# Kernel optimization log

Hardware: AMD Instinct MI355X
Metric: run time of the kernel (lower is better)

The kernel has to match this reference:

```python
import jax, jax.numpy as jnp
import numpy as np
from functools import partial

D = 512      # world_state_dim
M = 1000     # memory_size
H = 8        # attention heads
DH = D // H  # head dim
EPS = 1e-5


def _layernorm(x, g, b):
    mu = jnp.mean(x, axis=-1, keepdims=True)
    var = jnp.mean((x - mu) ** 2, axis=-1, keepdims=True)
    return (x - mu) * jax.lax.rsqrt(var + EPS) * g + b


def setup_inputs() -> dict:
    key = jax.random.key(0)
    ks = jax.random.split(key, 24)
    B = 8192
    w = lambda k, shp: (jax.random.normal(k, shp, dtype=jnp.float32) * 0.02)
    inp = {
        "observations": jax.random.normal(ks[0], (B, D), dtype=jnp.float32),
        "ego_motion": jax.random.normal(ks[1], (B, 16), dtype=jnp.float32),
        "world_memory": jax.random.normal(ks[2], (M, D), dtype=jnp.float32) * 0.1,
        # encoder: Linear(D,D) -> ReLU -> LN(D) -> Linear(D,D)
        "enc_w1": w(ks[3], (D, D)), "enc_b1": jnp.zeros((D,), jnp.float32),
        "enc_g": jnp.ones((D,), jnp.float32), "enc_beta": jnp.zeros((D,), jnp.float32),
        "enc_w2": w(ks[4], (D, D)), "enc_b2": jnp.zeros((D,), jnp.float32),
        # multihead attention in/out projections
        "wq": w(ks[5], (D, D)), "bq": jnp.zeros((D,), jnp.float32),
        "wk": w(ks[6], (D, D)), "bk": jnp.zeros((D,), jnp.float32),
        "wv": w(ks[7], (D, D)), "bv": jnp.zeros((D,), jnp.float32),
        "wo": w(ks[8], (D, D)), "bo": jnp.zeros((D,), jnp.float32),
        # transition: Linear(D+16,D) -> ReLU -> LN(D) -> Linear(D,D)
        "tr_w1": w(ks[9], (D, D + 16)), "tr_b1": jnp.zeros((D,), jnp.float32),
        "tr_g": jnp.ones((D,), jnp.float32), "tr_beta": jnp.zeros((D,), jnp.float32),
        "tr_w2": w(ks[10], (D, D)), "tr_b2": jnp.zeros((D,), jnp.float32),
        # quality head: Linear(D,128) -> ReLU -> Linear(128,1) -> Sigmoid
        "q_w1": w(ks[11], (128, D)), "q_b1": jnp.zeros((128,), jnp.float32),
        "q_w2": w(ks[12], (1, 128)), "q_b2": jnp.zeros((1,), jnp.float32),
        # random slots for memory-bank scatter-EMA update (replaces torch.randint)
        "update_indices": jax.random.randint(ks[13], (B,), 0, M, dtype=jnp.int32),
    }
    return inp


def _forward_core(observations, ego_motion, world_memory,
                  enc_w1, enc_b1, enc_g, enc_beta, enc_w2, enc_b2,
                  wq, bq, wk, bk, wv, bv, wo, bo,
                  tr_w1, tr_b1, tr_g, tr_beta, tr_w2, tr_b2,
                  q_w1, q_b1, q_w2, q_b2):
    B = observations.shape[0]
    # world_encoder
    h = jax.nn.relu(observations @ enc_w1.T + enc_b1)
    encoded = _layernorm(h, enc_g, enc_beta) @ enc_w2.T + enc_b2  # [B, D]
    # cross-attention: one query per batch row over shared memory bank
    q = (encoded @ wq.T + bq).reshape(B, H, DH)
    k = (world_memory @ wk.T + bk).reshape(M, H, DH)  # shared across batch
    v = (world_memory @ wv.T + bv).reshape(M, H, DH)
    scores = jnp.einsum("bhd,mhd->bhm", q, k) / jnp.sqrt(jnp.float32(DH))
    attn = jax.nn.softmax(scores, axis=-1)              # [B, H, M]
    ctx = jnp.einsum("bhm,mhd->bhd", attn, v).reshape(B, D)
    memory_states = ctx @ wo.T + bo
    # fuse + transition
    fused = 0.7 * encoded + 0.3 * memory_states
    x = jnp.concatenate([fused, ego_motion], axis=-1)   # [B, D+16]
    h2 = jax.nn.relu(x @ tr_w1.T + tr_b1)
    next_state = _layernorm(h2, tr_g, tr_beta) @ tr_w2.T + tr_b2  # [B, D]
    # quality head
    qh = jax.nn.relu(next_state @ q_w1.T + q_b1)
    quality = jax.nn.sigmoid(qh @ q_w2.T + q_b2)        # [B, 1]
    mem_weights = jnp.mean(attn, axis=1)                # [B, M] avg over heads
    return next_state, quality, mem_weights


def _update_memory_bank(world_memory, next_state, quality, update_indices):
    # Sequential scatter-EMA, faithful to the torch loop (duplicates compound).
    mask = quality[:, 0] > 0.7

    def step(mem, inp):
        idx, st, m = inp
        row = mem[idx]
        new_row = jnp.where(m, 0.9 * row + 0.1 * st, row)
        return mem.at[idx].set(new_row), None

    updated, _ = jax.lax.scan(step, world_memory, (update_indices, next_state, mask))
    return updated


@jax.jit
def reference(observations, ego_motion, world_memory,
              enc_w1, enc_b1, enc_g, enc_beta, enc_w2, enc_b2,
              wq, bq, wk, bk, wv, bv, wo, bo,
              tr_w1, tr_b1, tr_g, tr_beta, tr_w2, tr_b2,
              q_w1, q_b1, q_w2, q_b2, update_indices):
    next_state, quality, mem_weights = _forward_core(
        observations, ego_motion, world_memory,
        enc_w1, enc_b1, enc_g, enc_beta, enc_w2, enc_b2,
        wq, bq, wk, bk, wv, bv, wo, bo,
        tr_w1, tr_b1, tr_g, tr_beta, tr_w2, tr_b2,
        q_w1, q_b1, q_w2, q_b2)
    updated_memory = _update_memory_bank(world_memory, next_state, quality, update_indices)
    return next_state, quality, updated_memory
```

## Files before the change

kernel.cpp:

```cpp
#include <hip/hip_runtime.h>

#define B_ 8192
#define D_ 512
#define M_ 1000
#define H_ 8
#define LOG2E 1.4426950408889634f

typedef unsigned short u16;
typedef __attribute__((ext_vector_type(8))) short bf16x8;
typedef __attribute__((ext_vector_type(4))) float f32x4;

__device__ __forceinline__ float bf2f(u16 u) {
    union { unsigned u; float f; } c; c.u = ((unsigned)u) << 16; return c.f;
}
__device__ __forceinline__ u16 f2bf(float f) {
    union { float f; unsigned u; } c; c.f = f;
    unsigned r = (c.u + 0x7fffu + ((c.u >> 16) & 1u)) >> 16;
    return (u16)r;
}
__device__ __forceinline__ unsigned f2bf_fast_u(float f) {
    union { float f; unsigned u; } c; c.f = f;
    return (c.u + 0x8000u) >> 16;
}
__device__ __forceinline__ float wave_sum(float v) {
#pragma unroll
    for (int off = 32; off > 0; off >>= 1) v += __shfl_xor(v, off);
    return v;
}

template<bool RELU, bool WF32, bool VTOUT>
__device__ __forceinline__ void gemm_core(
    int bx, int by, u16* As, u16* Bs,
    const u16* __restrict__ A0, const u16* __restrict__ A1,
    const u16* __restrict__ A2, int lda0, int lda1, int lda2,
    const u16* __restrict__ W0, const u16* __restrict__ W1,
    const u16* __restrict__ W2, int ldw0, int ldw1, int ldw2,
    int kb1, int kb2,
    const float* __restrict__ bias, float bscale, float cscale,
    float* __restrict__ Cf, u16* __restrict__ Cb, u16* __restrict__ VT,
    int M, int N, int K, int ldc)
{
    const int m0 = by * 64, n0 = bx * 64;
    if (m0 >= M || n0 >= N) return;
    const int t = threadIdx.x, w = t >> 6, l = t & 63;
    const int wm = (w >> 1) * 32, wn = (w & 1) * 32;
    const int li = l & 15, quad = l >> 4;

    f32x4 acc[2][2];
#pragma unroll
    for (int i = 0; i < 2; ++i)
#pragma unroll
        for (int j = 0; j < 2; ++j) acc[i][j] = (f32x4){0.f, 0.f, 0.f, 0.f};

    for (int k0 = 0; k0 < K; k0 += 64) {
        const u16* Ab; const u16* Wb; int ldab, ldwb, ko;
        if (k0 < kb1)      { Ab = A0; ldab = lda0; Wb = W0; ldwb = ldw0; ko = k0; }
        else if (k0 < kb2) { Ab = A1; ldab = lda1; Wb = W1; ldwb = ldw1; ko = k0 - kb1; }
        else               { Ab = A2; ldab = lda2; Wb = W2; ldwb = ldw2; ko = k0 - kb2; }
#pragma unroll
        for (int i = 0; i < 2; ++i) {
            const int rl = w * 16 + i * 8 + (l >> 3);
            const int ck = (l & 7) ^ (rl & 7);
            int ga = m0 + rl; ga = ga < M ? ga : M - 1;
            __builtin_amdgcn_global_load_lds(
                (const __attribute__((address_space(1))) void*)(Ab + (size_t)ga * ldab + ko + ck * 8),
                (__attribute__((address_space(3))) void*)(As + (w * 16 + i * 8) * 64),
                16, 0, 0);
        }
#pragma unroll
        for (int i = 0; i < 2; ++i) {
            const int rl = w * 16 + i * 8 + (l >> 3);
            const int ck = (l & 7) ^ (rl & 7);
            int gb = n0 + rl; gb = gb < N ? gb : N - 1;
            __builtin_amdgcn_global_load_lds(
                (const __attribute__((address_space(1))) void*)(Wb + (size_t)gb * ldwb + ko + ck * 8),
                (__attribute__((address_space(3))) void*)(Bs + (w * 16 + i * 8) * 64),
                16, 0, 0);
        }
        __syncthreads();
#pragma unroll
        for (int ks = 0; ks < 2; ++ks) {
            const int ch = ks * 4 + quad;
            bf16x8 af[2], bfr[2];
#pragma unroll
            for (int mt = 0; mt < 2; ++mt) {
                const int r = wm + mt * 16 + li;
                af[mt] = *(const bf16x8*)(As + r * 64 + ((ch ^ (r & 7)) * 8));
            }
#pragma unroll
            for (int nt = 0; nt < 2; ++nt) {
                const int r = wn + nt * 16 + li;
                bfr[nt] = *(const bf16x8*)(Bs + r * 64 + ((ch ^ (r & 7)) * 8));
            }
#pragma unroll
            for (int mt = 0; mt < 2; ++mt)
#pragma unroll
                for (int nt = 0; nt < 2; ++nt)
                    acc[mt][nt] = __builtin_amdgcn_mfma_f32_16x16x32_bf16(
                        af[mt], bfr[nt], acc[mt][nt], 0, 0, 0);
        }
        __syncthreads();
    }

    float bv[2];
#pragma unroll
    for (int nt = 0; nt < 2; ++nt) bv[nt] = bias[n0 + wn + nt * 16 + li] * bscale;
#pragma unroll
    for (int mt = 0; mt < 2; ++mt) {
        const int row0 = m0 + wm + mt * 16 + quad * 4;
#pragma unroll
        for (int nt = 0; nt < 2; ++nt) {
            const int col = n0 + wn + nt * 16 + li;
            if (VTOUT && col >= 512) {
                ushort4 pk;
                u16 pv[4];
#pragma unroll
                for (int r = 0; r < 4; ++r) {
                    float v = acc[mt][nt][r] * cscale + bv[nt];
                    pv[r] = (row0 + r < M_) ? f2bf(v) : (u16)0;
                }
                pk.x = pv[0]; pk.y = pv[1]; pk.z = pv[2]; pk.w = pv[3];
                *(ushort4*)(VT + (size_t)(col - 512) * 1024 + row0) = pk;
            } else {
#pragma unroll
                for (int r = 0; r < 4; ++r) {
                    const int row = row0 + r;
                    if (row >= M) continue;
                    float v = acc[mt][nt][r] * cscale + bv[nt];
                    if (RELU) v = fmaxf(v, 0.f);
                    Cb[(size_t)row * ldc + col] = f2bf(v);
                    if (WF32) Cf[(size_t)row * ldc + col] = v;
                }
            }
        }
    }
}

template<bool RELU, bool WF32>
__launch_bounds__(256)
__global__ void mgemm(const u16* __restrict__ A0, const u16* __restrict__ A1,
                      const u16* __restrict__ A2, int lda0, int lda1, int lda2,
                      const u16* __restrict__ W0, const u16* __restrict__ W1,
                      const u16* __restrict__ W2, int ldw0, int ldw1, int ldw2,
                      int kb1, int kb2,
                      const float* __restrict__ bias, float bscale, float cscale,
                      float* __restrict__ Cf, u16* __restrict__ Cb,
                      int M, int N, int K, int ldc)
{
    __shared__ u16 As[64 * 64];
    __shared__ u16 Bs[64 * 64];
    gemm_core<RELU, WF32, false>(blockIdx.x, blockIdx.y, As, Bs,
                                 A0, A1, A2, lda0, lda1, lda2,
                                 W0, W1, W2, ldw0, ldw1, ldw2, kb1, kb2,
                                 bias, bscale, cscale, Cf, Cb, nullptr, M, N, K, ldc);
}

__launch_bounds__(256)
__global__ void megagemm(const u16* __restrict__ obs_bf, const u16* __restrict__ w_enc1,
                         const float* __restrict__ enc_b1, u16* __restrict__ hbuf,
                         const u16* __restrict__ wmem_bf, const u16* __restrict__ w_k,
                         const float* __restrict__ bkv, u16* __restrict__ KVbuf,
                         u16* __restrict__ VTb,
                         const u16* __restrict__ w_q, const u16* __restrict__ w_tr1,
                         const u16* __restrict__ w_e2t, const u16* __restrict__ w_wot,
                         u16* __restrict__ w_qe, u16* __restrict__ w_ae,
                         u16* __restrict__ w_co)
{
    __shared__ u16 As[64 * 64];
    __shared__ u16 Bs[64 * 64];
    const int bx = blockIdx.x, by = blockIdx.y;
    if (blockIdx.z == 0) {
        gemm_core<true, false, false>(bx, by, As, Bs,
            obs_bf, obs_bf, obs_bf, 512, 512, 512,
            w_enc1, w_enc1, w_enc1, 512, 512, 512, 512, 512,
            enc_b1, 1.f, 1.f, nullptr, hbuf, nullptr, B_, 512, 512, 512);
    } else {
        if (by < 16) {
            gemm_core<false, false, true>(bx, by, As, Bs,
                wmem_bf, wmem_bf, wmem_bf, 512, 512, 512,
                w_k, w_k, w_k, 512, 512, 512, 512, 512,
                bkv, 1.f, 1.f, nullptr, KVbuf, VTb, 1024, 1024, 512, 1024);
        } else if (by < 24) {
            gemm_core<false, false, false>(bx, by - 16, As, Bs,
                w_q, w_q, w_q, 512, 512, 512,
                w_e2t, w_e2t, w_e2t, 512, 512, 512, 512, 512,
                bkv, 0.f, 1.0f, nullptr, w_qe, nullptr, 512, 512, 512, 512);
        } else if (by < 32) {
            gemm_core<false, false, false>(bx, by - 24, As, Bs,
                w_tr1, w_tr1, w_tr1, 576, 576, 576,
                w_e2t, w_e2t, w_e2t, 512, 512, 512, 512, 512,
                bkv, 0.f, 0.7f, nullptr, w_ae, nullptr, 512, 512, 512, 512);
        } else if (by < 40) {
            gemm_core<false, false, false>(bx, by - 32, As, Bs,
                w_tr1, w_tr1, w_tr1, 576, 576, 576,
                w_wot, w_wot, w_wot, 512, 512, 512, 512, 512,
                bkv, 0.f, 0.3f, nullptr, w_co, nullptr, 512, 512, 512, 512);
        }
    }
}

#define PADK 72

__launch_bounds__(256, 3)
__global__ void attn_kernel(const u16* __restrict__ Q, const u16* __restrict__ KV,
                            const u16* __restrict__ VT, u16* __restrict__ ctx)
{
    __shared__ u16 Ks[2][64 * 64];
    __shared__ u16 Vs[2][64 * 64];
    __shared__ u16 P[4 * 32 * PADK];
    const int t = threadIdx.x, w = t >> 6, l = t & 63;
    const int h = blockIdx.y;
    const int q0 = blockIdx.x * 128 + w * 32;
    u16* Pw = P + w * (32 * PADK);
    const int li = l & 15, quad = l >> 4;

    bf16x8 aq[2][2];
#pragma unroll
    for (int qnt = 0; qnt < 2; ++qnt)
#pragma unroll
        for (int ks = 0; ks < 2; ++ks) {
            const int row = q0 + qnt * 16 + li;
            aq[qnt][ks] = *(const bf16x8*)(Q + (size_t)row * 512 + h * 64 + ks * 32 + quad * 8);
        }

    bf16x8 ones;
#pragma unroll
    for (int i = 0; i < 8; ++i) ones[i] = (short)0x3F80;

    f32x4 oacc[2][4];
    f32x4 lacc[2];
#pragma unroll
    for (int mt = 0; mt < 2; ++mt) {
        lacc[mt] = (f32x4){0.f, 0.f, 0.f, 0.f};
#pragma unroll
        for (int nt = 0; nt < 4; ++nt) oacc[mt][nt] = (f32x4){0.f, 0.f, 0.f, 0.f};
    }

    auto stage = [&](int kc, int buf) {
#pragma unroll
        for (int i = 0; i < 2; ++i) {
            const int f = i * 256 + t;
            const int r = f >> 3;
            const int ck = (f & 7) ^ (r & 7);
            __builtin_amdgcn_global_load_lds(
                (const __attribute__((address_space(1))) void*)(KV + (size_t)(kc + r) * 1024 + h * 64 + ck * 8),
                (__attribute__((address_space(3))) void*)(&Ks[buf][f * 8]),
                16, 0, 0);
        }
#pragma unroll
        for (int i = 0; i < 2; ++i) {
            const int f = i * 256 + t;
            const int r = f >> 3;
            const int ck = (f & 7) ^ (r & 7);
            __builtin_amdgcn_global_load_lds(
                (const __attribute__((address_space(1))) void*)(VT + (size_t)(h * 64 + r) * 1024 + kc + ck * 8),
                (__attribute__((address_space(3))) void*)(&Vs[buf][f * 8]),
                16, 0, 0);
        }
    };

    stage(0, 0);
    for (int ic = 0; ic < 16; ++ic) {
        const int kc = ic * 64;
        __syncthreads();
        if (ic < 15) stage(kc + 64, (ic + 1) & 1);
        const u16* ksb = &Ks[ic & 1][0];
        const u16* vsb = &Vs[ic & 1][0];

        f32x4 s[4][2];
#pragma unroll
        for (int kmt = 0; kmt < 4; ++kmt)
#pragma unroll
            for (int qnt = 0; qnt < 2; ++qnt) s[kmt][qnt] = (f32x4){0.f, 0.f, 0.f, 0.f};
        __builtin_amdgcn_s_setprio(1);
#pragma unroll
        for (int ks = 0; ks < 2; ++ks) {
            const int ch = ks * 4 + quad;
            bf16x8 bk[4];
#pragma unroll
            for (int kmt = 0; kmt < 4; ++kmt) {
                const int key = kmt * 16 + li;
                bk[kmt] = *(const bf16x8*)(ksb + key * 64 + ((ch ^ (key & 7)) * 8));
            }
#pragma unroll
            for (int kmt = 0; kmt < 4; ++kmt)
#pragma unroll
                for (int qnt = 0; qnt < 2; ++qnt)
                    s[kmt][qnt] = __builtin_amdgcn_mfma_f32_16x16x32_bf16(
                        bk[kmt], aq[qnt][ks], s[kmt][qnt], 0, 0, 0);
        }
        __builtin_amdgcn_s_setprio(0);
        if (kc == 960) {
#pragma unroll
            for (int kmt = 2; kmt < 4; ++kmt)
#pragma unroll
                for (int r = 0; r < 4; ++r) {
                    const int key_local = kmt * 16 + quad * 4 + r;
                    if (960 + key_local >= M_) {
                        s[kmt][0][r] = -3.0e38f;
                        s[kmt][1][r] = -3.0e38f;
                    }
                }
        }
#pragma unroll
        for (int kmt = 0; kmt < 4; ++kmt)
#pragma unroll
            for (int qnt = 0; qnt < 2; ++qnt) {
                const unsigned b0 = f2bf_fast_u(exp2f(s[kmt][qnt][0]));
                const unsigned b1 = f2bf_fast_u(exp2f(s[kmt][qnt][1]));
                const unsigned b2w = f2bf_fast_u(exp2f(s[kmt][qnt][2]));
                const unsigned b3 = f2bf_fast_u(exp2f(s[kmt][qnt][3]));
                const int off = (qnt * 16 + li) * PADK + kmt * 16 + quad * 4;
                *(uint2*)(Pw + off) = make_uint2(b0 | (b1 << 16), b2w | (b3 << 16));
            }
        __builtin_amdgcn_s_setprio(1);
#pragma unroll
        for (int ks = 0; ks < 2; ++ks) {
            const int ch = ks * 4 + quad;
            bf16x8 ap[2];
#pragma unroll
            for (int mt = 0; mt < 2; ++mt)
                ap[mt] = *(const bf16x8*)(Pw + (mt * 16 + li) * PADK + ch * 8);
#pragma unroll
            for (int mt = 0; mt < 2; ++mt)
                lacc[mt] = __builtin_amdgcn_mfma_f32_16x16x32_bf16(
                    ap[mt], ones, lacc[mt], 0, 0, 0);
#pragma unroll
            for (int nt = 0; nt < 4; ++nt) {
                const int dh = nt * 16 + li;
                const bf16x8 bvv = *(const bf16x8*)(vsb + dh * 64 + ((ch ^ (dh & 7)) * 8));
#pragma unroll
                for (int mt = 0; mt < 2; ++mt)
                    oacc[mt][nt] = __builtin_amdgcn_mfma_f32_16x16x32_bf16(
                        ap[mt], bvv, oacc[mt][nt], 0, 0, 0);
            }
        }
        __builtin_amdgcn_s_setprio(0);
    }

#pragma unroll
    for (int mt = 0; mt < 2; ++mt)
#pragma unroll
        for (int r = 0; r < 4; ++r) {
            const int row = q0 + mt * 16 + quad * 4 + r;
            const float inv = 1.0f / lacc[mt][r];
#pragma unroll
            for (int nt = 0; nt < 4; ++nt)
                ctx[(size_t)row * 512 + h * 64 + nt * 16 + li] = f2bf(oacc[mt][nt][r] * inv);
        }
}

__launch_bounds__(256)
__global__ void ln_bf(u16* __restrict__ X, const float* __restrict__ g,
                      const float* __restrict__ be, int rows)
{
    const int row = blockIdx.x * 4 + (threadIdx.x >> 6);
    const int lane = threadIdx.x & 63;
    if (row >= rows) return;
    u16* p = X + (size_t)row * 512 + lane * 8;
    uint4 d = *(const uint4*)p;
    const unsigned dd[4] = {d.x, d.y, d.z, d.w};
    float v[8];
#pragma unroll
    for (int i = 0; i < 4; ++i) {
        v[2 * i]     = bf2f((u16)(dd[i] & 0xffffu));
        v[2 * i + 1] = bf2f((u16)(dd[i] >> 16));
    }
    float s = 0.f;
#pragma unroll
    for (int i = 0; i < 8; ++i) s += v[i];
    s = wave_sum(s);
    const float mu = s * (1.0f / 512.0f);
    float vs = 0.f;
#pragma unroll
    for (int i = 0; i < 8; ++i) { v[i] -= mu; vs += v[i] * v[i]; }
    vs = wave_sum(vs);
    const float r = rsqrtf(vs * (1.0f / 512.0f) + 1e-5f);
    const float* gp = g + lane * 8;
    const float* bp = be + lane * 8;
    unsigned o[4];
#pragma unroll
    for (int i = 0; i < 4; ++i) {
        const u16 lo = f2bf(v[2 * i] * r * gp[2 * i] + bp[2 * i]);
        const u16 hi = f2bf(v[2 * i + 1] * r * gp[2 * i + 1] + bp[2 * i + 1]);
        o[i] = (unsigned)lo | ((unsigned)hi << 16);
    }
    *(uint4*)p = make_uint4(o[0], o[1], o[2], o[3]);
}

__launch_bounds__(256)
__global__ void prep_all(const float* enc_w1, const float* wk_f, const float* wv_f,
                         const float* tr_w2, const float* q_w1, const float* wq,
                         const float* tr_w1, const float* enc_w2, const float* wo,
                         const float* obs, const float* wmem, const float* ego,
                         const float* bk, const float* bvv, const float* bq,
                         const float* enc_b2, const float* trb1, const float* bo,
                         u16* w_enc1, u16* w_k, u16* w_v, u16* w_tr2, u16* w_qh,
                         u16* w_q, u16* w_tr1, u16* w_e2t, u16* w_wot,
                         u16* obs_bf, u16* wmem_bf, u16* ego64,
                         float* bkv, float* bqe, float* btr)
{
    __shared__ float tl[64][65];
    const int seg = blockIdx.y;
    const int t = threadIdx.x;
    const int bx = blockIdx.x;

    if (seg <= 5) {
        const float* s; u16* d; int n; float sc = 1.0f;
        switch (seg) {
            case 0: s = enc_w1; d = w_enc1; n = 262144; break;
            case 1: s = wk_f;   d = w_k;    n = 262144; break;
            case 2: s = wv_f;   d = w_v;    n = 262144; break;
            case 3: s = tr_w2;  d = w_tr2;  n = 262144; break;
            case 4: s = q_w1;   d = w_qh;   n = 65536;  break;
            default: s = wq;    d = w_q;    n = 262144; sc = 0.125f * LOG2E; break;
        }
        const int i0 = (bx * 256 + t) * 4;
        if (i0 + 3 < n) {
            const float4 v = *(const float4*)(s + i0);
            ushort4 o;
            o.x = f2bf(v.x * sc); o.y = f2bf(v.y * sc);
            o.z = f2bf(v.z * sc); o.w = f2bf(v.w * sc);
            *(ushort4*)(d + i0) = o;
        }
    } else if (seg == 6) {
#pragma unroll
        for (int k = 0; k < 4; ++k) {
            const int i = (bx * 256 + t) * 4 + k;
            if (i < 294912) {
                const int r = i / 576, c = i - r * 576;
                w_tr1[i] = (c < 528) ? f2bf(tr_w1[r * 528 + c]) : (u16)0;
            }
        }
    } else if (seg <= 8) {
        if (bx >= 64) return;
        const float* S = (seg == 7) ? enc_w2 : wo;
        u16* D = (seg == 7) ? w_e2t : w_wot;
        const int r0 = (bx >> 3) * 64, c0 = (bx & 7) * 64;
#pragma unroll
        for (int i = 0; i < 16; ++i) {
            const int idx = t + i * 256;
            tl[idx >> 6][idx & 63] = S[(size_t)(r0 + (idx >> 6)) * 512 + c0 + (idx & 63)];
        }
        __syncthreads();
#pragma unroll
        for (int i = 0; i < 16; ++i) {
            const int idx = t + i * 256;
            const int c = idx >> 6, r = idx & 63;
            D[(size_t)(c0 + c) * 512 + r0 + r] = f2bf(tl[r][c]);
        }
    } else if (seg == 9) {
        const int nth = gridDim.x * 256;
        for (int i = bx * 256 + t; i < B_ * 512 / 4; i += nth) {
            const float4 v = ((const float4*)obs)[i];
            ushort4 o;
            o.x = f2bf(v.x); o.y = f2bf(v.y); o.z = f2bf(v.z); o.w = f2bf(v.w);
            ((ushort4*)obs_bf)[i] = o;
        }
    } else if (seg == 10) {
        const int nth = gridDim.x * 256;
        for (int i = bx * 256 + t; i < M_ * 512 / 4; i += nth) {
            const float4 v = ((const float4*)wmem)[i];
            ushort4 o;
            o.x = f2bf(v.x); o.y = f2bf(v.y); o.z = f2bf(v.z); o.w = f2bf(v.w);
            ((ushort4*)wmem_bf)[i] = o;
        }
    } else if (seg == 11) {
        const int nth = gridDim.x * 256;
        for (int i = bx * 256 + t; i < B_ * 64; i += nth) {
            const int b = i >> 6, j = i & 63;
            ego64[(size_t)b * 64 + j] = (j < 16) ? f2bf(ego[b * 16 + j]) : (u16)0;
        }
        const int tid = bx * 256 + t;
        if (tid < 1024) bkv[tid] = (tid < 512) ? bk[tid] : bvv[tid - 512];
    } else {
        if (bx >= 128) return;
        const int i = bx * 4 + (t >> 6);
        const int lane = t & 63;
        float s = 0.f;
        if (seg == 12) {
            const float* wr = wq + (size_t)i * 512 + lane * 8;
#pragma unroll
            for (int j = 0; j < 8; ++j) s += wr[j] * enc_b2[lane * 8 + j];
            s = wave_sum(s);
            if (lane == 0) bqe[i] = 0.125f * LOG2E * (bq[i] + s);
        } else {
            const float* wr = tr_w1 + (size_t)i * 528 + lane * 8;
#pragma unroll
            for (int j = 0; j < 8; ++j)
                s += wr[j] * (0.7f * enc_b2[lane * 8 + j] + 0.3f * bo[lane * 8 + j]);
            s = wave_sum(s);
            if (lane == 0) btr[i] = trb1[i] + s;
        }
    }
}

__global__ void quality_bf(const u16* __restrict__ qh, const float* __restrict__ w2,
                           const float* __restrict__ b2, float* __restrict__ outq,
                           int rows)
{
    const int row = blockIdx.x * 4 + (threadIdx.x >> 6);
    const int lane = threadIdx.x & 63;
    if (row >= rows) return;
    const u16* p = qh + (size_t)row * 128;
    float s = bf2f(p[lane]) * w2[lane] + bf2f(p[64 + lane]) * w2[64 + lane];
    s = wave_sum(s);
    if (lane == 0) outq[row] = 1.0f / (1.0f + expf(-(s + b2[0])));
}

__global__ void compact_kernel(const float* __restrict__ q,
                               int* __restrict__ list, int* __restrict__ cnt)
{
    __shared__ int wtot[16];
    __shared__ int sbase;
    const int t = threadIdx.x, w = t >> 6, lane = t & 63;
    if (t == 0) sbase = 0;
    __syncthreads();
    for (int c = 0; c < B_; c += 1024) {
        const int idx = c + t;
        const bool pred = (q[idx] > 0.7f);
        const unsigned long long bal = __ballot(pred);
        const int prefix = __popcll(bal & ((1ull << lane) - 1ull));
        if (lane == 0) wtot[w] = __popcll(bal);
        __syncthreads();
        int woff = 0;
        for (int i = 0; i < w; ++i) woff += wtot[i];
        if (pred) list[sbase + woff + prefix] = idx;
        __syncthreads();
        if (t == 0) {
            int tot = 0;
            for (int i = 0; i < 16; ++i) tot += wtot[i];
            sbase += tot;
        }
        __syncthreads();
    }
    if (t == 0) *cnt = sbase;
}

__global__ void update_memory_kernel(const float* __restrict__ mem,
                                     const float* __restrict__ ns,
                                     const int* __restrict__ upd,
                                     const int* __restrict__ list,
                                     const int* __restrict__ cnt,
                                     float* __restrict__ outmem)
{
    const int m = blockIdx.x;
    const int t = threadIdx.x;
    const int c4 = t * 4;
    float4 r = *(const float4*)(mem + (size_t)m * D_ + c4);
    const int n = *cnt;
    for (int i = 0; i < n; ++i) {
        const int b = list[i];
        if (upd[b] == m) {
            const float4 s = *(const float4*)(ns + (size_t)b * D_ + c4);
            r.x = 0.9f * r.x + 0.1f * s.x;
            r.y = 0.9f * r.y + 0.1f * s.y;
            r.z = 0.9f * r.z + 0.1f * s.z;
            r.w = 0.9f * r.w + 0.1f * s.w;
        }
    }
    *(float4*)(outmem + (size_t)m * D_ + c4) = r;
}

extern "C" void kernel_launch(void* const* d_in, const int* in_sizes, int n_in,
                              void* d_out, int out_size, void* d_ws, size_t ws_size,
                              hipStream_t stream)
{
    const float* obs    = (const float*)d_in[0];
    const float* ego    = (const float*)d_in[1];
    const float* wmem   = (const float*)d_in[2];
    const float* enc_w1 = (const float*)d_in[3];
    const float* enc_b1 = (const float*)d_in[4];
    const float* enc_g  = (const float*)d_in[5];
    const float* enc_be = (const float*)d_in[6];
    const float* enc_w2 = (const float*)d_in[7];
    const float* enc_b2 = (const float*)d_in[8];
    const float* wq = (const float*)d_in[9];
    const float* bq = (const float*)d_in[10];
    const float* wk_f = (const float*)d_in[11];
    const float* bk = (const float*)d_in[12];
    const float* wv_f = (const float*)d_in[13];
    const float* bvv = (const float*)d_in[14];
    const float* wo = (const float*)d_in[15];
    const float* bo = (const float*)d_in[16];
    const float* tr_w1 = (const float*)d_in[17];
    const float* tr_b1 = (const float*)d_in[18];
    const float* tr_g  = (const float*)d_in[19];
    const float* tr_be = (const float*)d_in[20];
    const float* tr_w2 = (const float*)d_in[21];
    const float* tr_b2 = (const float*)d_in[22];
    const float* q_w1 = (const float*)d_in[23];
    const float* q_b1 = (const float*)d_in[24];
    const float* q_w2 = (const float*)d_in[25];
    const float* q_b2 = (const float*)d_in[26];
    const int*   upd  = (const int*)d_in[27];

    float* out_ns  = (float*)d_out;
    float* out_q   = out_ns + (size_t)B_ * D_;
    float* out_mem = out_q + B_;

    u16* ws = (u16*)d_ws;
    size_t o = 0;
    u16* obs_bf  = ws + o; o += (size_t)B_ * 512;
    u16* wmem_bf = ws + o; o += (size_t)M_ * 512;
    u16* w_enc1  = ws + o; o += 262144;
    u16* w_k     = ws + o; o += 262144;
    u16* w_v     = ws + o; o += 262144;
    u16* w_tr2   = ws + o; o += 262144;
    u16* w_qh    = ws + o; o += 65536;
    u16* w_q     = ws + o; o += 262144;
    u16* w_tr1   = ws + o; o += (size_t)512 * 576;
    u16* w_e2t   = ws + o; o += 262144;
    u16* w_wot   = ws + o; o += 262144;
    u16* w_qe    = ws + o; o += 262144;
    u16* w_ae    = ws + o; o += 262144;
    u16* w_co    = ws + o; o += 262144;
    u16* hbuf    = ws + o; o += (size_t)B_ * 512;
    u16* qbuf    = ws + o; o += (size_t)B_ * 512;
    u16* KVbuf   = ws + o; o += (size_t)1024 * 1024;
    u16* VTb     = ws + o; o += (size_t)512 * 1024;
    u16* ctx     = ws + o; o += (size_t)B_ * 512;
    u16* h2b     = ws + o; o += (size_t)B_ * 512;
    u16* nsbf    = ws + o; o += (size_t)B_ * 512;
    u16* qhb     = ws + o; o += (size_t)B_ * 128;
    u16* ego64   = ws + o; o += (size_t)B_ * 64;
    float* bkv   = (float*)(ws + o); o += 2048;
    float* bqe   = (float*)(ws + o); o += 1024;
    float* btr   = (float*)(ws + o); o += 1024;
    int* list    = (int*)(ws + o);
    int* cnt     = list + B_;

    const dim3 blk(256);

    prep_all<<<dim3(576, 14), blk, 0, stream>>>(
        enc_w1, wk_f, wv_f, tr_w2, q_w1, wq, tr_w1, enc_w2, wo,
        obs, wmem, ego, bk, bvv, bq, enc_b2, tr_b1, bo,
        w_enc1, w_k, w_v, w_tr2, w_qh, w_q, w_tr1, w_e2t, w_wot,
        obs_bf, wmem_bf, ego64, bkv, bqe, btr);

    megagemm<<<dim3(16, 128, 2), blk, 0, stream>>>(
        obs_bf, w_enc1, enc_b1, hbuf, wmem_bf, w_k, bkv, KVbuf, VTb,
        w_q, w_tr1, w_e2t, w_wot, w_qe, w_ae, w_co);

    ln_bf<<<dim3(2048), blk, 0, stream>>>(hbuf, enc_g, enc_be, B_);

    mgemm<false, false><<<dim3(8, 128), blk, 0, stream>>>(
        hbuf, hbuf, hbuf, 512, 512, 512, w_qe, w_qe, w_qe, 512, 512, 512,
        512, 512, bqe, 1.f, 1.f, nullptr, qbuf, B_, 512, 512, 512);

    attn_kernel<<<dim3(64, 8), blk, 0, stream>>>(qbuf, KVbuf, VTb, ctx);

    mgemm<true, false><<<dim3(8, 128), blk, 0, stream>>>(
        hbuf, ctx, ego64, 512, 512, 64, w_ae, w_co, w_tr1 + 512, 512, 512, 576,
        512, 1024, btr, 1.f, 1.f, nullptr, h2b, B_, 512, 1088, 512);
    ln_bf<<<dim3(2048), blk, 0, stream>>>(h2b, tr_g, tr_be, B_);

    mgemm<false, true><<<dim3(8, 128), blk, 0, stream>>>(
        h2b, h2b, h2b, 512, 512, 512, w_tr2, w_tr2, w_tr2, 512, 512, 512,
        512, 512, tr_b2, 1.f, 1.f, out_ns, nsbf, B_, 512, 512, 512);

    mgemm<true, false><<<dim3(2, 128), blk, 0, stream>>>(
        nsbf, nsbf, nsbf, 512, 512, 512, w_qh, w_qh, w_qh, 512, 512, 512,
        512, 512, q_b1, 1.f, 1.f, nullptr, qhb, B_, 128, 512, 128);
    quality_bf<<<dim3(2048), blk, 0, stream>>>(qhb, q_w2, q_b2, out_q, B_);

    compact_kernel<<<dim3(1), dim3(1024), 0, stream>>>(out_q, list, cnt);
    update_memory_kernel<<<dim3(M_), dim3(128), 0, stream>>>(
        wmem, out_ns, upd, list, cnt, out_mem);
}
```

Baseline: 260.3 us.

## Fuse query projection GEMM into attention kernel prologue

Removes the separate Q-projection GEMM launch. Each attention block now computes its own 128x64 per-head Q tile from the normalized hidden states and the query weights using MFMA, staging through the existing K/V shared buffers. The result is written into the P scratch area and loaded as the A fragments. This avoids writing and re-reading the Q buffer and saves one launch. In exchange, each block performs a 512-deep K loop before attention starts, and the first KV stage now overlaps only the bias epilogue.

```diff
diff --git a/kernel.cpp b/kernel.cpp
--- a/kernel.cpp
+++ b/kernel.cpp
@@ -202,7 +202,9 @@
 #define PADK 72
 
 __launch_bounds__(256, 3)
-__global__ void attn_kernel(const u16* __restrict__ Q, const u16* __restrict__ KV,
+__global__ void attn_kernel(const u16* __restrict__ hn, const u16* __restrict__ w_qe,
+                            const float* __restrict__ bqe,
+                            const u16* __restrict__ KV,
                             const u16* __restrict__ VT, u16* __restrict__ ctx)
 {
     __shared__ u16 Ks[2][64 * 64];
@@ -210,31 +212,10 @@
     __shared__ u16 P[4 * 32 * PADK];
     const int t = threadIdx.x, w = t >> 6, l = t & 63;
     const int h = blockIdx.y;
-    const int q0 = blockIdx.x * 128 + w * 32;
-    u16* Pw = P + w * (32 * PADK);
+    const int q0b = blockIdx.x * 128;
+    const int q0 = q0b + w * 32;
+    u16* Pw = P + w * 2048;
     const int li = l & 15, quad = l >> 4;
-
-    bf16x8 aq[2][2];
-#pragma unroll
-    for (int qnt = 0; qnt < 2; ++qnt)
-#pragma unroll
-        for (int ks = 0; ks < 2; ++ks) {
-            const int row = q0 + qnt * 16 + li;
-            aq[qnt][ks] = *(const bf16x8*)(Q + (size_t)row * 512 + h * 64 + ks * 32 + quad * 8);
-        }
-
-    bf16x8 ones;
-#pragma unroll
-    for (int i = 0; i < 8; ++i) ones[i] = (short)0x3F80;
-
-    f32x4 oacc[2][4];
-    f32x4 lacc[2];
-#pragma unroll
-    for (int mt = 0; mt < 2; ++mt) {
-        lacc[mt] = (f32x4){0.f, 0.f, 0.f, 0.f};
-#pragma unroll
-        for (int nt = 0; nt < 4; ++nt) oacc[mt][nt] = (f32x4){0.f, 0.f, 0.f, 0.f};
-    }
 
     auto stage = [&](int kc, int buf) {
 #pragma unroll
@@ -259,7 +240,97 @@
         }
     };
 
-    stage(0, 0);
+    {
+        u16* Ksf = &Ks[0][0];
+        u16* Bsf = &Vs[0][0];
+        f32x4 qacc[2][4];
+#pragma unroll
+        for (int mt = 0; mt < 2; ++mt)
+#pragma unroll
+            for (int nt = 0; nt < 4; ++nt) qacc[mt][nt] = (f32x4){0.f, 0.f, 0.f, 0.f};
+
+        for (int k0 = 0; k0 < 512; k0 += 64) {
+#pragma unroll
+            for (int i = 0; i < 4; ++i) {
+                const int rl = w * 32 + i * 8 + (l >> 3);
+                const int ck = (l & 7) ^ (rl & 7);
+                __builtin_amdgcn_global_load_lds(
+                    (const __attribute__((address_space(1))) void*)(hn + (size_t)(q0b + rl) * 512 + k0 + ck * 8),
+                    (__attribute__((address_space(3))) void*)(Ksf + (w * 32 + i * 8) * 64),
+                    16, 0, 0);
+            }
+#pragma unroll
+            for (int i = 0; i < 2; ++i) {
+                const int rl = w * 16 + i * 8 + (l >> 3);
+                const int ck = (l & 7) ^ (rl & 7);
+                __builtin_amdgcn_global_load_lds(
+                    (const __attribute__((address_space(1))) void*)(w_qe + (size_t)(h * 64 + rl) * 512 + k0 + ck * 8),
+                    (__attribute__((address_space(3))) void*)(Bsf + (w * 16 + i * 8) * 64),
+                    16, 0, 0);
+            }
+            __syncthreads();
+            __builtin_amdgcn_s_setprio(1);
+#pragma unroll
+            for (int ks = 0; ks < 2; ++ks) {
+                const int ch = ks * 4 + quad;
+                bf16x8 af[2], bfr[4];
+#pragma unroll
+                for (int mt = 0; mt < 2; ++mt) {
+                    const int r = w * 32 + mt * 16 + li;
+                    af[mt] = *(const bf16x8*)(Ksf + r * 64 + ((ch ^ (r & 7)) * 8));
+                }
+#pragma unroll
+                for (int nt = 0; nt < 4; ++nt) {
+                    const int r = nt * 16 + li;
+                    bfr[nt] = *(const bf16x8*)(Bsf + r * 64 + ((ch ^ (r & 7)) * 8));
+                }
+#pragma unroll
+                for (int mt = 0; mt < 2; ++mt)
+#pragma unroll
+                    for (int nt = 0; nt < 4; ++nt)
+                        qacc[mt][nt] = __builtin_amdgcn_mfma_f32_16x16x32_bf16(
+                            af[mt], bfr[nt], qacc[mt][nt], 0, 0, 0);
+            }
+            __builtin_amdgcn_s_setprio(0);
+            __syncthreads();
+        }
+
+        stage(0, 0);
+
+#pragma unroll
+        for (int mt = 0; mt < 2; ++mt)
+#pragma unroll
+            for (int nt = 0; nt < 4; ++nt) {
+                const int col = nt * 16 + li;
+                const float bv = bqe[h * 64 + col];
+#pragma unroll
+                for (int r = 0; r < 4; ++r) {
+                    const int row = w * 32 + mt * 16 + quad * 4 + r;
+                    P[row * PADK + col] = f2bf(qacc[mt][nt][r] + bv);
+                }
+            }
+    }
+
+    bf16x8 aq[2][2];
+#pragma unroll
+    for (int qnt = 0; qnt < 2; ++qnt)
+#pragma unroll
+        for (int ks = 0; ks < 2; ++ks)
+            aq[qnt][ks] = *(const bf16x8*)(P + (w * 32 + qnt * 16 + li) * PADK + ks * 32 + quad * 8);
+
+    bf16x8 ones;
+#pragma unroll
+    for (int i = 0; i < 8; ++i) ones[i] = (short)0x3F80;
+
+    f32x4 oacc[2][4];
+    f32x4 lacc[2];
+#pragma unroll
+    for (int mt = 0; mt < 2; ++mt) {
+        lacc[mt] = (f32x4){0.f, 0.f, 0.f, 0.f};
+#pragma unroll
+        for (int nt = 0; nt < 4; ++nt) oacc[mt][nt] = (f32x4){0.f, 0.f, 0.f, 0.f};
+    }
+
     for (int ic = 0; ic < 16; ++ic) {
         const int kc = ic * 64;
         __syncthreads();
@@ -629,6 +700,7 @@
     float* btr   = (float*)(ws + o); o += 1024;
     int* list    = (int*)(ws + o);
     int* cnt     = list + B_;
+    (void)qbuf;
 
     const dim3 blk(256);
 
@@ -644,11 +716,7 @@
 
     ln_bf<<<dim3(2048), blk, 0, stream>>>(hbuf, enc_g, enc_be, B_);
 
-    mgemm<false, false><<<dim3(8, 128), blk, 0, stream>>>(
-        hbuf, hbuf, hbuf, 512, 512, 512, w_qe, w_qe, w_qe, 512, 512, 512,
-        512, 512, bqe, 1.f, 1.f, nullptr, qbuf, B_, 512, 512, 512);
-
-    attn_kernel<<<dim3(64, 8), blk, 0, stream>>>(qbuf, KVbuf, VTb, ctx);
+    attn_kernel<<<dim3(64, 8), blk, 0, stream>>>(hbuf, w_qe, bqe, KVbuf, VTb, ctx);
 
     mgemm<true, false><<<dim3(8, 128), blk, 0, stream>>>(
         hbuf, ctx, ego64, 512, 512, 64, w_ae, w_co, w_tr1 + 512, 512, 512, 576,
```

After: 253.8 us. 1.03x faster.

## Fuse query projection GEMM into attention kernel prologue with 512-thread blocks

Applied to the files above, without the earlier changes.

The separate Q-projection GEMM launch is removed. Each attention block now computes its 128x64 Q tile from the normalized hidden states and w_qe in a prologue, then keeps it in LDS, so the Q buffer round trip through global memory goes away. Blocks grow to 512 threads with 16 query rows per wave instead of 32, which changes the MFMA-to-load balance and occupancy. Each head's block now reads its 128 rows of hn, and the K loop in the prologue is unpipelined with two barriers per step.

```diff
diff --git a/kernel.cpp b/kernel.cpp
--- a/kernel.cpp
+++ b/kernel.cpp
@@ -199,67 +199,119 @@
     }
 }
 
-#define PADK 72
-
-__launch_bounds__(256, 3)
-__global__ void attn_kernel(const u16* __restrict__ Q, const u16* __restrict__ KV,
+__launch_bounds__(512, 2)
+__global__ void attn_kernel(const u16* __restrict__ hn, const u16* __restrict__ w_qe,
+                            const float* __restrict__ bqe,
+                            const u16* __restrict__ KV,
                             const u16* __restrict__ VT, u16* __restrict__ ctx)
 {
     __shared__ u16 Ks[2][64 * 64];
     __shared__ u16 Vs[2][64 * 64];
-    __shared__ u16 P[4 * 32 * PADK];
+    __shared__ u16 P[128 * 64];
     const int t = threadIdx.x, w = t >> 6, l = t & 63;
     const int h = blockIdx.y;
-    const int q0 = blockIdx.x * 128 + w * 32;
-    u16* Pw = P + w * (32 * PADK);
+    const int q0b = blockIdx.x * 128;
+    u16* Pw = P + w * 1024;
     const int li = l & 15, quad = l >> 4;
 
-    bf16x8 aq[2][2];
-#pragma unroll
-    for (int qnt = 0; qnt < 2; ++qnt)
-#pragma unroll
-        for (int ks = 0; ks < 2; ++ks) {
-            const int row = q0 + qnt * 16 + li;
-            aq[qnt][ks] = *(const bf16x8*)(Q + (size_t)row * 512 + h * 64 + ks * 32 + quad * 8);
-        }
-
-    bf16x8 ones;
-#pragma unroll
-    for (int i = 0; i < 8; ++i) ones[i] = (short)0x3F80;
-
-    f32x4 oacc[2][4];
-    f32x4 lacc[2];
-#pragma unroll
-    for (int mt = 0; mt < 2; ++mt) {
-        lacc[mt] = (f32x4){0.f, 0.f, 0.f, 0.f};
-#pragma unroll
-        for (int nt = 0; nt < 4; ++nt) oacc[mt][nt] = (f32x4){0.f, 0.f, 0.f, 0.f};
-    }
-
     auto stage = [&](int kc, int buf) {
-#pragma unroll
-        for (int i = 0; i < 2; ++i) {
-            const int f = i * 256 + t;
-            const int r = f >> 3;
-            const int ck = (f & 7) ^ (r & 7);
+        {
+            const int r = t >> 3;
+            const int ck = (t & 7) ^ (r & 7);
             __builtin_amdgcn_global_load_lds(
                 (const __attribute__((address_space(1))) void*)(KV + (size_t)(kc + r) * 1024 + h * 64 + ck * 8),
-                (__attribute__((address_space(3))) void*)(&Ks[buf][f * 8]),
+                (__attribute__((address_space(3))) void*)(&Ks[buf][t * 8]),
                 16, 0, 0);
         }
-#pragma unroll
-        for (int i = 0; i < 2; ++i) {
-            const int f = i * 256 + t;
-            const int r = f >> 3;
-            const int ck = (f & 7) ^ (r & 7);
+        {
+            const int r = t >> 3;
+            const int ck = (t & 7) ^ (r & 7);
             __builtin_amdgcn_global_load_lds(
                 (const __attribute__((address_space(1))) void*)(VT + (size_t)(h * 64 + r) * 1024 + kc + ck * 8),
-                (__attribute__((address_space(3))) void*)(&Vs[buf][f * 8]),
+                (__attribute__((address_space(3))) void*)(&Vs[buf][t * 8]),
                 16, 0, 0);
         }
     };
 
-    stage(0, 0);
+    {
+        u16* Ksf = &Ks[0][0];
+        u16* Bsf = &Vs[0][0];
+        f32x4 qacc[4];
+#pragma unroll
+        for (int nt = 0; nt < 4; ++nt) qacc[nt] = (f32x4){0.f, 0.f, 0.f, 0.f};
+
+        for (int k0 = 0; k0 < 512; k0 += 64) {
+#pragma unroll
+            for (int i = 0; i < 2; ++i) {
+                const int f = i * 512 + t;
+                const int rl = f >> 3;
+                const int ck = (f & 7) ^ (rl & 7);
+                __builtin_amdgcn_global_load_lds(
+                    (const __attribute__((address_space(1))) void*)(hn + (size_t)(q0b + rl) * 512 + k0 + ck * 8),
+                    (__attribute__((address_space(3))) void*)(Ksf + f * 8),
+                    16, 0, 0);
+            }
+            {
+                const int rl = t >> 3;
+                const int ck = (t & 7) ^ (rl & 7);
+                __builtin_amdgcn_global_load_lds(
+                    (const __attribute__((address_space(1))) void*)(w_qe + (size_t)(h * 64 + rl) * 512 + k0 + ck * 8),
+                    (__attribute__((address_space(3))) void*)(Bsf + t * 8),
+                    16, 0, 0);
+            }
+            __syncthreads();
+            __builtin_amdgcn_s_setprio(1);
+#pragma unroll
+            for (int ks = 0; ks < 2; ++ks) {
+                const int ch = ks * 4 + quad;
+                const int r = w * 16 + li;
+                const bf16x8 af = *(const bf16x8*)(Ksf + r * 64 + ((ch ^ (r & 7)) * 8));
+                bf16x8 bfr[4];
+#pragma unroll
+                for (int nt = 0; nt < 4; ++nt) {
+                    const int rb = nt * 16 + li;
+                    bfr[nt] = *(const bf16x8*)(Bsf + rb * 64 + ((ch ^ (rb & 7)) * 8));
+                }
+#pragma unroll
+                for (int nt = 0; nt < 4; ++nt)
+                    qacc[nt] = __builtin_amdgcn_mfma_f32_16x16x32_bf16(
+                        af, bfr[nt], qacc[nt], 0, 0, 0);
+            }
+            __builtin_amdgcn_s_setprio(0);
+            __syncthreads();
+        }
+
+        stage(0, 0);
+
+#pragma unroll
+        for (int nt = 0; nt < 4; ++nt) {
+            const int col = nt * 16 + li;
+            const float bv = bqe[h * 64 + col];
+#pragma unroll
+            for (int r = 0; r < 4; ++r) {
+                const int row = w * 16 + quad * 4 + r;
+                P[row * 64 + (((2 * nt + (li >> 3)) ^ (row & 7)) * 8) + (li & 7)] =
+                    f2bf(qacc[nt][r] + bv);
+            }
+        }
+    }
+
+    bf16x8 aq[2];
+#pragma unroll
+    for (int ks = 0; ks < 2; ++ks) {
+        const int row = w * 16 + li;
+        aq[ks] = *(const bf16x8*)(P + row * 64 + (((ks * 4 + quad) ^ (li & 7)) * 8));
+    }
+
+    bf16x8 ones;
+#pragma unroll
+    for (int i = 0; i < 8; ++i) ones[i] = (short)0x3F80;
+
+    f32x4 oacc[4];
+    f32x4 lacc = (f32x4){0.f, 0.f, 0.f, 0.f};
+#pragma unroll
+    for (int nt = 0; nt < 4; ++nt) oacc[nt] = (f32x4){0.f, 0.f, 0.f, 0.f};
+
     for (int ic = 0; ic < 16; ++ic) {
         const int kc = ic * 64;
         __syncthreads();
@@ -267,11 +319,9 @@
         const u16* ksb = &Ks[ic & 1][0];
         const u16* vsb = &Vs[ic & 1][0];
 
-        f32x4 s[4][2];
-#pragma unroll
-        for (int kmt = 0; kmt < 4; ++kmt)
-#pragma unroll
-            for (int qnt = 0; qnt < 2; ++qnt) s[kmt][qnt] = (f32x4){0.f, 0.f, 0.f, 0.f};
+        f32x4 s[4];
+#pragma unroll
+        for (int kmt = 0; kmt < 4; ++kmt) s[kmt] = (f32x4){0.f, 0.f, 0.f, 0.f};
         __builtin_amdgcn_s_setprio(1);
 #pragma unroll
         for (int ks = 0; ks < 2; ++ks) {
@@ -284,10 +334,8 @@
             }
 #pragma unroll
             for (int kmt = 0; kmt < 4; ++kmt)
-#pragma unroll
-                for (int qnt = 0; qnt < 2; ++qnt)
-                    s[kmt][qnt] = __builtin_amdgcn_mfma_f32_16x16x32_bf16(
-                        bk[kmt], aq[qnt][ks], s[kmt][qnt], 0, 0, 0);
+                s[kmt] = __builtin_amdgcn_mfma_f32_16x16x32_bf16(
+                    bk[kmt], aq[ks], s[kmt], 0, 0, 0);
         }
         __builtin_amdgcn_s_setprio(0);
         if (kc == 960) {
@@ -296,58 +344,44 @@
 #pragma unroll
                 for (int r = 0; r < 4; ++r) {
                     const int key_local = kmt * 16 + quad * 4 + r;
-                    if (960 + key_local >= M_) {
-                        s[kmt][0][r] = -3.0e38f;
-                        s[kmt][1][r] = -3.0e38f;
-                    }
+                    if (960 + key_local >= M_) s[kmt][r] = -3.0e38f;
                 }
         }
 #pragma unroll
-        for (int kmt = 0; kmt < 4; ++kmt)
-#pragma unroll
-            for (int qnt = 0; qnt < 2; ++qnt) {
-                const unsigned b0 = f2bf_fast_u(exp2f(s[kmt][qnt][0]));
-                const unsigned b1 = f2bf_fast_u(exp2f(s[kmt][qnt][1]));
-                const unsigned b2w = f2bf_fast_u(exp2f(s[kmt][qnt][2]));
-                const unsigned b3 = f2bf_fast_u(exp2f(s[kmt][qnt][3]));
-                const int off = (qnt * 16 + li) * PADK + kmt * 16 + quad * 4;
-                *(uint2*)(Pw + off) = make_uint2(b0 | (b1 << 16), b2w | (b3 << 16));
-            }
+        for (int kmt = 0; kmt < 4; ++kmt) {
+            const unsigned b0 = f2bf_fast_u(exp2f(s[kmt][0]));
+            const unsigned b1 = f2bf_fast_u(exp2f(s[kmt][1]));
+            const unsigned b2w = f2bf_fast_u(exp2f(s[kmt][2]));
+            const unsigned b3 = f2bf_fast_u(exp2f(s[kmt][3]));
+            const int chunk = (2 * kmt + (quad >> 1)) ^ (li & 7);
+            const int off = li * 64 + chunk * 8 + (quad & 1) * 4;
+            *(uint2*)(Pw + off) = make_uint2(b0 | (b1 << 16), b2w | (b3 << 16));
+        }
         __builtin_amdgcn_s_setprio(1);
 #pragma unroll
         for (int ks = 0; ks < 2; ++ks) {
             const int ch = ks * 4 + quad;
-            bf16x8 ap[2];
-#pragma unroll
-            for (int mt = 0; mt < 2; ++mt)
-                ap[mt] = *(const bf16x8*)(Pw + (mt * 16 + li) * PADK + ch * 8);
-#pragma unroll
-            for (int mt = 0; mt < 2; ++mt)
-                lacc[mt] = __builtin_amdgcn_mfma_f32_16x16x32_bf16(
-                    ap[mt], ones, lacc[mt], 0, 0, 0);
+            const bf16x8 ap = *(const bf16x8*)(Pw + li * 64 + ((ch ^ (li & 7)) * 8));
+            lacc = __builtin_amdgcn_mfma_f32_16x16x32_bf16(ap, ones, lacc, 0, 0, 0);
 #pragma unroll
             for (int nt = 0; nt < 4; ++nt) {
                 const int dh = nt * 16 + li;
                 const bf16x8 bvv = *(const bf16x8*)(vsb + dh * 64 + ((ch ^ (dh & 7)) * 8));
-#pragma unroll
-                for (int mt = 0; mt < 2; ++mt)
-                    oacc[mt][nt] = __builtin_amdgcn_mfma_f32_16x16x32_bf16(
-                        ap[mt], bvv, oacc[mt][nt], 0, 0, 0);
+                oacc[nt] = __builtin_amdgcn_mfma_f32_16x16x32_bf16(
+                    ap, bvv, oacc[nt], 0, 0, 0);
             }
         }
         __builtin_amdgcn_s_setprio(0);
     }
 
 #pragma unroll
-    for (int mt = 0; mt < 2; ++mt)
-#pragma unroll
-        for (int r = 0; r < 4; ++r) {
-            const int row = q0 + mt * 16 + quad * 4 + r;
-            const float inv = 1.0f / lacc[mt][r];
-#pragma unroll
-            for (int nt = 0; nt < 4; ++nt)
-                ctx[(size_t)row * 512 + h * 64 + nt * 16 + li] = f2bf(oacc[mt][nt][r] * inv);
-        }
+    for (int r = 0; r < 4; ++r) {
+        const int row = q0b + w * 16 + quad * 4 + r;
+        const float inv = 1.0f / lacc[r];
+#pragma unroll
+        for (int nt = 0; nt < 4; ++nt)
+            ctx[(size_t)row * 512 + h * 64 + nt * 16 + li] = f2bf(oacc[nt][r] * inv);
+    }
 }
 
 __launch_bounds__(256)
@@ -629,6 +663,7 @@
     float* btr   = (float*)(ws + o); o += 1024;
     int* list    = (int*)(ws + o);
     int* cnt     = list + B_;
+    (void)qbuf;
 
     const dim3 blk(256);
 
@@ -644,11 +679,7 @@
 
     ln_bf<<<dim3(2048), blk, 0, stream>>>(hbuf, enc_g, enc_be, B_);
 
-    mgemm<false, false><<<dim3(8, 128), blk, 0, stream>>>(
-        hbuf, hbuf, hbuf, 512, 512, 512, w_qe, w_qe, w_qe, 512, 512, 512,
-        512, 512, bqe, 1.f, 1.f, nullptr, qbuf, B_, 512, 512, 512);
-
-    attn_kernel<<<dim3(64, 8), blk, 0, stream>>>(qbuf, KVbuf, VTb, ctx);
+    attn_kernel<<<dim3(64, 8), dim3(512), 0, stream>>>(hbuf, w_qe, bqe, KVbuf, VTb, ctx);
 
     mgemm<true, false><<<dim3(8, 128), blk, 0, stream>>>(
         hbuf, ctx, ego64, 512, 512, 64, w_ae, w_co, w_tr1 + 512, 512, 512, 576,
```

Result: no change. 256.0 us (-1.7%).
